# Kernel tuning notes

Hardware: AMD Instinct MI355X
Metric: run time of the kernel (lower is better)

## Reference

```python
import jax, jax.numpy as jnp
import numpy as np

N = 50000      # nodes per type
E = 800000     # edges per relation
CIN = 64       # in_channels
H, O = 2, 32   # heads, out_channels
HID = H * O    # hidden
EC = 16        # edge_channels


def setup_inputs() -> dict:
    key = jax.random.key(0)
    ks = jax.random.split(key, 30)
    f = lambda i, shape, s=0.1: jax.random.normal(ks[i], shape, dtype=jnp.float32) * s
    inp = {
        'x_a': f(0, (N, CIN), 1.0), 'x_b': f(1, (N, CIN), 1.0),
        'edge_attr1': f(2, (E, EC), 1.0), 'edge_attr2': f(3, (E, EC), 1.0),
        'Wq_a': f(4, (CIN, HID)), 'Wk_a': f(5, (CIN, HID)), 'Wv_a': f(6, (CIN, HID)),
        'Wq_b': f(7, (CIN, HID)), 'Wk_b': f(8, (CIN, HID)), 'Wv_b': f(9, (CIN, HID)),
        'emb_a': f(10, (HID,)), 'emb_b': f(11, (HID,)),
        'rel1': f(12, (HID,)), 'rel2': f(13, (HID,)),
        'We': f(14, (EC, HID)), 'a_attn': f(15, (4 * O,)),
        'Wo_a': f(16, (HID, O)), 'bo_a': f(17, (O,)),
        'Wo_b': f(18, (HID, O)), 'bo_b': f(19, (O,)),
        'Wr_a': f(20, (CIN, O)), 'Wr_b': f(21, (CIN, O)),
        'row1': jax.random.randint(ks[22], (E,), 0, N),
        'col1': jax.random.randint(ks[23], (E,), 0, N),
        'row2': jax.random.randint(ks[24], (E,), 0, N),
        'col2': jax.random.randint(ks[25], (E,), 0, N),
    }
    return inp


def _edge_softmax(scores, col, num_dst):
    # softmax over incoming edges of each destination node; scores: [E, H]
    m = jax.ops.segment_max(scores, col, num_segments=num_dst)      # [N, H]
    ex = jnp.exp(scores - m[col])
    s = jax.ops.segment_sum(ex, col, num_segments=num_dst)          # [N, H]
    return ex / s[col]


def _relation(q_dst, k_src, v_src, emb_src, emb_dst, rel_emb, edge_bias,
              row, col, a_attn, num_dst):
    eb = edge_bias                                                  # [E, H, O]
    qd = q_dst[col] + emb_dst.reshape(1, H, O)
    ks = k_src[row] + emb_src.reshape(1, H, O)
    rb = jnp.broadcast_to(rel_emb.reshape(1, H, O), qd.shape)
    attn_in = jnp.concatenate([qd, ks, rb, eb], axis=-1)            # [E, H, 4O]
    scores = jnp.einsum('ehd,d->eh', jnp.tanh(attn_in), a_attn)    # [E, H]
    w = _edge_softmax(scores, col, num_dst)                         # [E, H]
    msg = v_src[row] + rel_emb.reshape(1, H, O) + eb                # [E, H, O]
    agg = jax.ops.segment_sum(msg * w[..., None], col, num_segments=num_dst)
    return agg.reshape(num_dst, H * O)


def reference(x_a, x_b, edge_attr1, edge_attr2,
              Wq_a, Wk_a, Wv_a, Wq_b, Wk_b, Wv_b,
              emb_a, emb_b, rel1, rel2, We, a_attn,
              Wo_a, bo_a, Wo_b, bo_b, Wr_a, Wr_b,
              row1, col1, row2, col2):
    q_a = (x_a @ Wq_a).reshape(-1, H, O)
    k_a = (x_a @ Wk_a).reshape(-1, H, O)
    v_a = (x_a @ Wv_a).reshape(-1, H, O)
    q_b = (x_b @ Wq_b).reshape(-1, H, O)
    k_b = (x_b @ Wk_b).reshape(-1, H, O)
    v_b = (x_b @ Wv_b).reshape(-1, H, O)

    # relation r1: a -> b
    eb1 = (edge_attr1 @ We).reshape(-1, H, O)
    out_b = _relation(q_b, k_a, v_a, emb_a, emb_b, rel1, eb1, row1, col1, a_attn, N)
    # relation r2: b -> a
    eb2 = (edge_attr2 @ We).reshape(-1, H, O)
    out_a = _relation(q_a, k_b, v_b, emb_b, emb_a, rel2, eb2, row2, col2, a_attn, N)

    fin_a = out_a @ Wo_a + bo_a + x_a @ Wr_a                        # [N, O]
    fin_b = out_b @ Wo_b + bo_b + x_b @ Wr_b                        # [N, O]
    return jnp.concatenate([fin_a, fin_b], axis=0)                  # [2N, O]
```

## Files before the change

### kernel.cpp

```cpp
#include <hip/hip_runtime.h>
#include <hip/hip_bf16.h>

typedef __hip_bfloat16 bf16;
typedef __attribute__((ext_vector_type(8))) short short8;
typedef __attribute__((ext_vector_type(4))) float float4v;

static __device__ __forceinline__ float b2f(bf16 x) { return __bfloat162float(x); }

static __device__ __forceinline__ float ldf(const void* p, size_t i, int f32) {
    return f32 ? ((const float*)p)[i] : b2f(((const bf16*)p)[i]);
}
static __device__ __forceinline__ void stf(void* p, size_t i, int f32, float v) {
    if (f32) ((float*)p)[i] = v;
    else     ((bf16*)p)[i] = __float2bfloat16(v);
}
static __device__ __forceinline__ unsigned short f2bf_bits(float f) {
    bf16 h = __float2bfloat16(f);
    return *(unsigned short*)&h;
}

static __device__ __forceinline__ float fast_tanh(float x) {
    float t = __expf(2.f * x);
    return 1.f - 2.f * __builtin_amdgcn_rcpf(t + 1.f);
}

static __device__ __forceinline__ void load_ea16(const void* ea, size_t e, int f32, float* er) {
    if (f32) {
        const float4* p = (const float4*)((const float*)ea + e * 16);
        #pragma unroll
        for (int q = 0; q < 4; ++q) {
            float4 v = p[q];
            er[4*q] = v.x; er[4*q+1] = v.y; er[4*q+2] = v.z; er[4*q+3] = v.w;
        }
    } else {
        const uint4* p = (const uint4*)((const bf16*)ea + e * 16);
        #pragma unroll
        for (int q = 0; q < 2; ++q) {
            uint4 u = p[q];
            er[8*q+0] = __uint_as_float(u.x << 16);
            er[8*q+1] = __uint_as_float(u.x & 0xffff0000u);
            er[8*q+2] = __uint_as_float(u.y << 16);
            er[8*q+3] = __uint_as_float(u.y & 0xffff0000u);
            er[8*q+4] = __uint_as_float(u.z << 16);
            er[8*q+5] = __uint_as_float(u.z & 0xffff0000u);
            er[8*q+6] = __uint_as_float(u.w << 16);
            er[8*q+7] = __uint_as_float(u.w & 0xffff0000u);
        }
    }
}

__global__ void detect_kernel(const unsigned short* __restrict__ a, int* __restrict__ flag)
{
    __shared__ int cnt;
    if (threadIdx.x == 0) cnt = 0;
    __syncthreads();
    unsigned e = (a[threadIdx.x] >> 7) & 0xFF;
    if (e < 100 || e > 133) atomicAdd(&cnt, 1);
    __syncthreads();
    if (threadIdx.x == 0) *flag = (cnt >= 16) ? 1 : 0;
}

__global__ __launch_bounds__(256) void prep_small_kernel(
    const void* __restrict__ W0, const void* __restrict__ W1,
    const void* __restrict__ W2, const void* __restrict__ W3,
    const void* __restrict__ W4, const void* __restrict__ W5,
    const void* __restrict__ Wr_a, const void* __restrict__ Wr_b,
    const void* __restrict__ We,
    const void* __restrict__ Wo_a, const void* __restrict__ Wo_b,
    const void* __restrict__ rel1, const void* __restrict__ rel2,
    const void* __restrict__ a_attn, const int* __restrict__ flagp,
    unsigned short* __restrict__ wt,
    float* __restrict__ M1, float* __restrict__ c321,
    float* __restrict__ M2, float* __restrict__ c322,
    float* __restrict__ cvals)
{
    const int f32 = *flagp;
    const int bid = blockIdx.x;
    if (bid < 6) {
        const void* src;
        switch (bid) {
            case 0: src = W0; break; case 1: src = W1; break; case 2: src = W2; break;
            case 3: src = W3; break; case 4: src = W4; break; default: src = W5; break;
        }
        unsigned short* dst = wt + bid * 4096;
        for (int i = threadIdx.x; i < 4096; i += 256) {
            int c = i >> 6, j = i & 63;
            dst[j * 64 + c] = f2bf_bits(ldf(src, c * 64 + j, f32));
        }
    } else if (bid < 8) {
        const void* src = (bid == 6) ? Wr_a : Wr_b;
        unsigned short* dst = wt + 24576 + (bid - 6) * 2048;
        for (int i = threadIdx.x; i < 2048; i += 256) {
            int c = i >> 5, j = i & 31;
            dst[j * 64 + c] = f2bf_bits(ldf(src, c * 32 + j, f32));
        }
    } else {
        const int sel = bid - 8;
        const void* Wo  = sel ? Wo_a : Wo_b;
        const void* rel = sel ? rel2 : rel1;
        float* M   = sel ? M2 : M1;
        float* c32 = sel ? c322 : c321;
        const int t = threadIdx.x;
        for (int i = t; i < 1024; i += 256) {
            int m = i >> 5, j = i & 31;
            int h = m >> 4, c = m & 15;
            float s = 0.f;
            for (int jj = 0; jj < 32; ++jj)
                s += ldf(We, c * 64 + h * 32 + jj, f32) * ldf(Wo, (size_t)(h * 32 + jj) * 32 + j, f32);
            M[m * 32 + j] = s;
        }
        if (t < 32) {
            float s2 = 0.f;
            for (int ch = 0; ch < 64; ++ch)
                s2 += ldf(rel, ch, f32) * ldf(Wo, (size_t)ch * 32 + t, f32);
            c32[t] = s2;
        }
        if (t == 252 || t == 253) {
            int h = t - 252;
            float s3 = 0.f;
            for (int l = 0; l < 32; ++l)
                s3 += tanhf(ldf(rel, h * 32 + l, f32)) * ldf(a_attn, 64 + l, f32);
            cvals[sel * 2 + h] = s3;
        }
    }
}

__global__ __launch_bounds__(256) void node_prep_mfma_kernel(
    const void* __restrict__ x_a, const void* __restrict__ x_b,
    const unsigned short* __restrict__ wt,
    const void* __restrict__ emb_a, const void* __restrict__ emb_b,
    const void* __restrict__ a_attn, const int* __restrict__ flagp,
    unsigned short* __restrict__ v_a, unsigned short* __restrict__ v_b,
    float* __restrict__ r_a, float* __restrict__ r_b,
    float* __restrict__ sq_a, float* __restrict__ sk_a,
    float* __restrict__ sq_b, float* __restrict__ sk_b,
    int n_nodes, int tiles)
{
    const int f32 = *flagp;
    const int wave_id = blockIdx.x * 4 + (threadIdx.x >> 6);
    if (wave_id >= 2 * tiles) return;
    const int type = (wave_id >= tiles);
    const int tile = type ? (wave_id - tiles) : wave_id;

    const void* xp = type ? x_b : x_a;
    const unsigned short* wq = wt + (type ? 3 * 4096 : 0);
    const unsigned short* wk = wq + 4096;
    const unsigned short* wv = wk + 4096;
    const unsigned short* wr = wt + 24576 + (type ? 2048 : 0);
    const void* embp = type ? emb_b : emb_a;
    unsigned short* v_out = type ? v_b : v_a;
    float*  r_out  = type ? r_b : r_a;
    float2* sq_out = (float2*)(type ? sq_b : sq_a);
    float2* sk_out = (float2*)(type ? sk_b : sk_a);

    const int lane = threadIdx.x & 63;
    const int ml   = lane & 15;
    const int g    = lane >> 4;
    const int g8   = g * 8;

    float embc[4], acq[4], ack[4];
    #pragma unroll
    for (int t = 0; t < 4; ++t) {
        int colt = t * 16 + ml;
        embc[t] = ldf(embp, colt, f32);
        acq[t]  = ldf(a_attn, colt & 31, f32);
        ack[t]  = ldf(a_attn, 32 + (colt & 31), f32);
    }

    short8 Bq[4][2], Bk[4][2], Bv[4][2], Br[2][2];
    #pragma unroll
    for (int t = 0; t < 4; ++t) {
        const int rowo = (t * 16 + ml) * 64;
        #pragma unroll
        for (int kh = 0; kh < 2; ++kh) {
            const int o = rowo + kh * 32 + g8;
            Bq[t][kh] = __builtin_bit_cast(short8, *(const uint4*)(wq + o));
            Bk[t][kh] = __builtin_bit_cast(short8, *(const uint4*)(wk + o));
            Bv[t][kh] = __builtin_bit_cast(short8, *(const uint4*)(wv + o));
            if (t < 2)
                Br[t][kh] = __builtin_bit_cast(short8, *(const uint4*)(wr + o));
        }
    }

    const int n0 = tile << 4;
    int nr = n0 + ml; if (nr > n_nodes - 1) nr = n_nodes - 1;
    short8 A0, A1;
    if (f32) {
        const float4* xr = (const float4*)((const float*)xp + (size_t)nr * 64);
        float4 f0 = xr[2*g], f1 = xr[2*g+1], f2 = xr[8+2*g], f3 = xr[9+2*g];
        short8 a0, a1;
        a0[0]=(short)f2bf_bits(f0.x); a0[1]=(short)f2bf_bits(f0.y);
        a0[2]=(short)f2bf_bits(f0.z); a0[3]=(short)f2bf_bits(f0.w);
        a0[4]=(short)f2bf_bits(f1.x); a0[5]=(short)f2bf_bits(f1.y);
        a0[6]=(short)f2bf_bits(f1.z); a0[7]=(short)f2bf_bits(f1.w);
        a1[0]=(short)f2bf_bits(f2.x); a1[1]=(short)f2bf_bits(f2.y);
        a1[2]=(short)f2bf_bits(f2.z); a1[3]=(short)f2bf_bits(f2.w);
        a1[4]=(short)f2bf_bits(f3.x); a1[5]=(short)f2bf_bits(f3.y);
        a1[6]=(short)f2bf_bits(f3.z); a1[7]=(short)f2bf_bits(f3.w);
        A0 = a0; A1 = a1;
    } else {
        const uint4* xr = (const uint4*)((const bf16*)xp + (size_t)nr * 64);
        A0 = __builtin_bit_cast(short8, xr[g]);
        A1 = __builtin_bit_cast(short8, xr[4 + g]);
    }

    float4v accq[4], acck[4], accv[4], accr[2];
    #pragma unroll
    for (int t = 0; t < 4; ++t) {
        float4v z = {0.f, 0.f, 0.f, 0.f};
        accq[t] = z; acck[t] = z; accv[t] = z;
        if (t < 2) accr[t] = z;
    }
    #pragma unroll
    for (int t = 0; t < 4; ++t) {
        accq[t] = __builtin_amdgcn_mfma_f32_16x16x32_bf16(A0, Bq[t][0], accq[t], 0, 0, 0);
        accq[t] = __builtin_amdgcn_mfma_f32_16x16x32_bf16(A1, Bq[t][1], accq[t], 0, 0, 0);
        acck[t] = __builtin_amdgcn_mfma_f32_16x16x32_bf16(A0, Bk[t][0], acck[t], 0, 0, 0);
        acck[t] = __builtin_amdgcn_mfma_f32_16x16x32_bf16(A1, Bk[t][1], acck[t], 0, 0, 0);
        accv[t] = __builtin_amdgcn_mfma_f32_16x16x32_bf16(A0, Bv[t][0], accv[t], 0, 0, 0);
        accv[t] = __builtin_amdgcn_mfma_f32_16x16x32_bf16(A1, Bv[t][1], accv[t], 0, 0, 0);
        if (t < 2) {
            accr[t] = __builtin_amdgcn_mfma_f32_16x16x32_bf16(A0, Br[t][0], accr[t], 0, 0, 0);
            accr[t] = __builtin_amdgcn_mfma_f32_16x16x32_bf16(A1, Br[t][1], accr[t], 0, 0, 0);
        }
    }

    #pragma unroll
    for (int t = 0; t < 4; ++t) {
        #pragma unroll
        for (int r = 0; r < 4; ++r) {
            int node = n0 + g * 4 + r;
            if (node < n_nodes) {
                v_out[(size_t)node * 64 + t * 16 + ml] = f2bf_bits(accv[t][r]);
                if (t < 2) r_out[(size_t)node * 32 + t * 16 + ml] = accr[t][r];
            }
        }
    }

    #pragma unroll
    for (int r = 0; r < 4; ++r) {
        float q0 = fast_tanh(accq[0][r] + embc[0]) * acq[0]
                 + fast_tanh(accq[1][r] + embc[1]) * acq[1];
        float q1 = fast_tanh(accq[2][r] + embc[2]) * acq[2]
                 + fast_tanh(accq[3][r] + embc[3]) * acq[3];
        float k0 = fast_tanh(acck[0][r] + embc[0]) * ack[0]
                 + fast_tanh(acck[1][r] + embc[1]) * ack[1];
        float k1 = fast_tanh(acck[2][r] + embc[2]) * ack[2]
                 + fast_tanh(acck[3][r] + embc[3]) * ack[3];
        #pragma unroll
        for (int o = 1; o < 16; o <<= 1) {
            q0 += __shfl_xor(q0, o, 64); q1 += __shfl_xor(q1, o, 64);
            k0 += __shfl_xor(k0, o, 64); k1 += __shfl_xor(k1, o, 64);
        }
        int node = n0 + g * 4 + r;
        if (ml == 0 && node < n_nodes) {
            sq_out[node] = make_float2(q0, q1);
            sk_out[node] = make_float2(k0, k1);
        }
    }
}

__global__ __launch_bounds__(256) void hist_kernel(
    const int* __restrict__ col1, const int* __restrict__ col2,
    int* __restrict__ cnt, int n_nodes, int num_e)
{
    const int sel = blockIdx.x & 1;
    const int bx  = blockIdx.x >> 1;
    const int* col = sel ? col2 : col1;
    const int rb = sel ? n_nodes : 0;
    int e = bx * 256 + threadIdx.x;
    if (e < num_e) atomicAdd(&cnt[rb + col[e]], 1);
}

__global__ __launch_bounds__(256) void scan1_kernel(const int* __restrict__ cnt,
                                                    int* __restrict__ partial, int n)
{
    __shared__ int wsum[4];
    int t = threadIdx.x;
    int i0 = blockIdx.x * 512 + 2 * t;
    int s = ((i0 < n) ? cnt[i0] : 0) + ((i0 + 1 < n) ? cnt[i0 + 1] : 0);
    #pragma unroll
    for (int o = 32; o; o >>= 1) s += __shfl_xor(s, o, 64);
    if ((t & 63) == 0) wsum[t >> 6] = s;
    __syncthreads();
    if (t == 0) partial[blockIdx.x] = wsum[0] + wsum[1] + wsum[2] + wsum[3];
}

__global__ void scan2_kernel(const int* __restrict__ partial, int* __restrict__ pp,
                             int* __restrict__ off, int nch, int noff)
{
    int lane = threadIdx.x;
    int running = 0;
    for (int base = 0; base < nch; base += 64) {
        int i = base + lane;
        int o = (i < nch) ? partial[i] : 0;
        int v = o;
        #pragma unroll
        for (int d = 1; d < 64; d <<= 1) {
            int u = __shfl_up(v, d, 64);
            if (lane >= d) v += u;
        }
        if (i < nch) pp[i] = running + v - o;
        running += __shfl(v, 63, 64);
    }
    if (lane == 0) off[noff] = running;
}

__global__ __launch_bounds__(256) void scan3_kernel(const int* __restrict__ cnt,
                                                    const int* __restrict__ pp,
                                                    int* __restrict__ off,
                                                    int* __restrict__ cursor, int n)
{
    __shared__ int tmp[256];
    int t = threadIdx.x;
    int i0 = blockIdx.x * 512 + 2 * t;
    int v0 = (i0 < n) ? cnt[i0] : 0;
    int v1 = (i0 + 1 < n) ? cnt[i0 + 1] : 0;
    int pair = v0 + v1;
    tmp[t] = pair;
    __syncthreads();
    for (int d = 1; d < 256; d <<= 1) {
        int x = (t >= d) ? tmp[t - d] : 0;
        __syncthreads();
        tmp[t] += x;
        __syncthreads();
    }
    int excl = tmp[t] - pair + pp[blockIdx.x];
    if (i0 < n)     { off[i0] = excl;          cursor[i0] = excl; }
    if (i0 + 1 < n) { off[i0 + 1] = excl + v0; cursor[i0 + 1] = excl + v0; }
}

__global__ __launch_bounds__(256) void edge_score_scatter_kernel(
    const void* __restrict__ ea1p, const void* __restrict__ ea2p,
    const void* __restrict__ We,
    const int* __restrict__ row1, const int* __restrict__ col1,
    const int* __restrict__ row2, const int* __restrict__ col2,
    const float* __restrict__ sq_bp, const float* __restrict__ sk_ap,
    const float* __restrict__ sq_ap, const float* __restrict__ sk_bp,
    const float* __restrict__ cvals, const void* __restrict__ a_attn,
    const int* __restrict__ flagp, int* __restrict__ cursor,
    uint4* __restrict__ payload, int n_nodes, int num_e)
{
    const int f32 = *flagp;
    const int sel = blockIdx.x & 1;
    const int bx  = blockIdx.x >> 1;
    const void* ea = sel ? ea2p : ea1p;
    const int* row = sel ? row2 : row1;
    const int* col = sel ? col2 : col1;
    const float* sq_dst = sel ? sq_ap : sq_bp;
    const float* sk_src = sel ? sk_bp : sk_ap;
    const int rb = sel ? n_nodes : 0;

    __shared__ float We_s[16 * 64];
    __shared__ float a3_s[32];
    for (int i = threadIdx.x; i < 16 * 64; i += 256) We_s[i] = ldf(We, i, f32);
    if (threadIdx.x < 32) a3_s[threadIdx.x] = ldf(a_attn, 96 + threadIdx.x, f32);
    const float c0 = cvals[sel * 2 + 0];
    const float c1 = cvals[sel * 2 + 1];
    __syncthreads();

    const int e0 = bx * 512 + threadIdx.x;
    const int e1 = e0 + 256;
    const bool v1e = (e1 < num_e);
    if (e0 >= num_e) return;

    float er0[16], er1[16];
    load_ea16(ea, (size_t)e0, f32, er0);
    if (v1e) load_ea16(ea, (size_t)e1, f32, er1);
    else {
        #pragma unroll
        for (int c = 0; c < 16; ++c) er1[c] = 0.f;
    }

    float acc00 = 0.f, acc01 = 0.f, acc10 = 0.f, acc11 = 0.f;
    #pragma unroll 1
    for (int jb = 0; jb < 64; jb += 16) {
        float t0[16], t1[16];
        #pragma unroll
        for (int jj = 0; jj < 16; ++jj) { t0[jj] = 0.f; t1[jj] = 0.f; }
        #pragma unroll
        for (int c = 0; c < 16; ++c) {
            #pragma unroll
            for (int jj = 0; jj < 16; ++jj) {
                float w = We_s[c * 64 + jb + jj];
                t0[jj] += er0[c] * w;
                t1[jj] += er1[c] * w;
            }
        }
        float p0 = 0.f, p1 = 0.f;
        #pragma unroll
        for (int jj = 0; jj < 16; ++jj) {
            float a = a3_s[(jb + jj) & 31];
            p0 += fast_tanh(t0[jj]) * a;
            p1 += fast_tanh(t1[jj]) * a;
        }
        if (jb & 32) { acc01 += p0; acc11 += p1; }
        else         { acc00 += p0; acc10 += p1; }
    }

    {
        int dc = col[e0], s = row[e0];
        float2 sqd = ((const float2*)sq_dst)[dc];
        float2 sks = ((const float2*)sk_src)[s];
        float s0 = fminf(30.f, fmaxf(-30.f, acc00 + sqd.x + sks.x + c0));
        float s1 = fminf(30.f, fmaxf(-30.f, acc01 + sqd.y + sks.y + c1));
        int pos = atomicAdd(&cursor[rb + dc], 1);
        uint4* rec = payload + (size_t)3 * pos;
        unsigned w0 = (unsigned)f2bf_bits(er0[0])  | ((unsigned)f2bf_bits(er0[1])  << 16);
        unsigned w1 = (unsigned)f2bf_bits(er0[2])  | ((unsigned)f2bf_bits(er0[3])  << 16);
        unsigned w2 = (unsigned)f2bf_bits(er0[4])  | ((unsigned)f2bf_bits(er0[5])  << 16);
        unsigned w3 = (unsigned)f2bf_bits(er0[6])  | ((unsigned)f2bf_bits(er0[7])  << 16);
        unsigned w4 = (unsigned)f2bf_bits(er0[8])  | ((unsigned)f2bf_bits(er0[9])  << 16);
        unsigned w5 = (unsigned)f2bf_bits(er0[10]) | ((unsigned)f2bf_bits(er0[11]) << 16);
        unsigned w6 = (unsigned)f2bf_bits(er0[12]) | ((unsigned)f2bf_bits(er0[13]) << 16);
        unsigned w7 = (unsigned)f2bf_bits(er0[14]) | ((unsigned)f2bf_bits(er0[15]) << 16);
        rec[0] = make_uint4((unsigned)s, __float_as_uint(__expf(s0)), __float_as_uint(__expf(s1)), 0u);
        rec[1] = make_uint4(w0, w1, w2, w3);
        rec[2] = make_uint4(w4, w5, w6, w7);
    }
    if (v1e) {
        int dc = col[e1], s = row[e1];
        float2 sqd = ((const float2*)sq_dst)[dc];
        float2 sks = ((const float2*)sk_src)[s];
        float s0 = fminf(30.f, fmaxf(-30.f, acc10 + sqd.x + sks.x + c0));
        float s1 = fminf(30.f, fmaxf(-30.f, acc11 + sqd.y + sks.y + c1));
        int pos = atomicAdd(&cursor[rb + dc], 1);
        uint4* rec = payload + (size_t)3 * pos;
        unsigned w0 = (unsigned)f2bf_bits(er1[0])  | ((unsigned)f2bf_bits(er1[1])  << 16);
        unsigned w1 = (unsigned)f2bf_bits(er1[2])  | ((unsigned)f2bf_bits(er1[3])  << 16);
        unsigned w2 = (unsigned)f2bf_bits(er1[4])  | ((unsigned)f2bf_bits(er1[5])  << 16);
        unsigned w3 = (unsigned)f2bf_bits(er1[6])  | ((unsigned)f2bf_bits(er1[7])  << 16);
        unsigned w4 = (unsigned)f2bf_bits(er1[8])  | ((unsigned)f2bf_bits(er1[9])  << 16);
        unsigned w5 = (unsigned)f2bf_bits(er1[10]) | ((unsigned)f2bf_bits(er1[11]) << 16);
        unsigned w6 = (unsigned)f2bf_bits(er1[12]) | ((unsigned)f2bf_bits(er1[13]) << 16);
        unsigned w7 = (unsigned)f2bf_bits(er1[14]) | ((unsigned)f2bf_bits(er1[15]) << 16);
        rec[0] = make_uint4((unsigned)s, __float_as_uint(__expf(s0)), __float_as_uint(__expf(s1)), 0u);
        rec[1] = make_uint4(w0, w1, w2, w3);
        rec[2] = make_uint4(w4, w5, w6, w7);
    }
}

__global__ __launch_bounds__(256) void agg_final_kernel(
    const uint4* __restrict__ payload, const int* __restrict__ off,
    const unsigned short* __restrict__ v_a, const unsigned short* __restrict__ v_b,
    const float* __restrict__ r_a, const float* __restrict__ r_b,
    const void* __restrict__ Wo_a, const void* __restrict__ Wo_b,
    const void* __restrict__ bo_a, const void* __restrict__ bo_b,
    const float* __restrict__ M1, const float* __restrict__ M2,
    const float* __restrict__ c321, const float* __restrict__ c322,
    const int* __restrict__ flagp, void* __restrict__ out,
    int n_nodes, int nbh)
{
    const int sel = blockIdx.x & 1;
    const int bx  = blockIdx.x >> 1;
    const unsigned short* v_src = sel ? v_b : v_a;
    const float* r_src = sel ? r_a : r_b;
    const void*  Wo    = sel ? Wo_a : Wo_b;
    const void*  bo    = sel ? bo_a : bo_b;
    const float* M     = sel ? M2 : M1;
    const float* c32   = sel ? c322 : c321;
    const int relbase  = sel ? n_nodes : 0;
    const size_t out_off = sel ? 0 : (size_t)n_nodes * 32;

    const int f32  = *flagp;
    const int lane = threadIdx.x & 63;
    const int wv   = threadIdx.x >> 6;
    const int j    = lane & 31;
    const int half = lane >> 5;
    const int c16  = lane & 15;
    const bool hi  = (lane >= 32);

    __shared__ float stage[4][96];

    float WoR[32], MR[16];
    const int cb = half * 32;
    #pragma unroll
    for (int cc = 0; cc < 32; ++cc)
        WoR[cc] = ldf(Wo, (size_t)(cb + cc) * 32 + j, f32);
    const int ub = half * 16;
    #pragma unroll
    for (int cc = 0; cc < 16; ++cc) MR[cc] = M[(ub + cc) * 32 + j];
    const float boR  = ldf(bo, j, f32);
    const float c32R = c32[j];

    const int stride = nbh * 4;
    const int iters  = (n_nodes + stride - 1) / stride;
    int d = bx * 4 + wv;

    for (int it = 0; it < iters; ++it, d += stride) {
        const bool valid = (d < n_nodes);
        const int dd  = valid ? d : (n_nodes - 1);
        const int idx = relbase + dd;
        const int b   = __builtin_amdgcn_readfirstlane(off[idx]);
        const int en  = __builtin_amdgcn_readfirstlane(off[idx + 1]);
        const int deg = en - b;

        const float rv = r_src[(size_t)dd * 32 + j];

        float den0 = 0.f, den1 = 0.f, y = 0.f, ua = 0.f;
        int k = b;
        #pragma unroll 1
        for (; k + 8 <= en; k += 8) {
            uint4 m[8];
            #pragma unroll
            for (int q = 0; q < 8; ++q) m[q] = payload[(size_t)3 * (k + q)];
            float ev[8];
            #pragma unroll
            for (int q = 0; q < 8; ++q) {
                const unsigned short* pq = (const unsigned short*)(payload + (size_t)3 * (k + q) + 1);
                ev[q] = __uint_as_float((unsigned)pq[c16] << 16);
            }
            float vv[8];
            #pragma unroll
            for (int q = 0; q < 8; ++q)
                vv[q] = __uint_as_float((unsigned)v_src[(size_t)m[q].x * 64 + lane] << 16);
            #pragma unroll
            for (int q = 0; q < 8; ++q) {
                float e0 = __uint_as_float(m[q].y), e1 = __uint_as_float(m[q].z);
                den0 += e0; den1 += e1;
                float xw = hi ? e1 : e0;
                y  = fmaf(xw, vv[q], y);
                ua = fmaf(xw, ev[q], ua);
            }
        }
        #pragma unroll 1
        for (; k < en; ++k) {
            uint4 mm = payload[(size_t)3 * k];
            const unsigned short* pq = (const unsigned short*)(payload + (size_t)3 * k + 1);
            float evs = __uint_as_float((unsigned)pq[c16] << 16);
            float vvs = __uint_as_float((unsigned)v_src[(size_t)mm.x * 64 + lane] << 16);
            float e0 = __uint_as_float(mm.y), e1 = __uint_as_float(mm.z);
            den0 += e0; den1 += e1;
            float xw = hi ? e1 : e0;
            y  = fmaf(xw, vvs, y);
            ua = fmaf(xw, evs, ua);
        }

        float inv0 = (deg > 0) ? __builtin_amdgcn_rcpf(den0) : 0.f;
        float inv1 = (deg > 0) ? __builtin_amdgcn_rcpf(den1) : 0.f;
        const float invh = hi ? inv1 : inv0;
        y  *= invh;
        ua *= invh;

        float* st = stage[wv];
        st[lane] = y;
        if ((lane & 31) < 16) st[64 + half * 16 + c16] = ua;
        __asm__ volatile("s_waitcnt lgkmcnt(0)" ::: "memory");

        float acc = 0.f;
        #pragma unroll
        for (int cc = 0; cc < 32; ++cc)
            acc = fmaf(st[cb + cc], WoR[cc], acc);
        #pragma unroll
        for (int cc = 0; cc < 16; ++cc)
            acc = fmaf(st[64 + ub + cc], MR[cc], acc);

        float other = __shfl(acc, lane ^ 32, 64);
        if (valid && lane < 32) {
            float o = acc + other + boR + rv + ((deg > 0) ? c32R : 0.f);
            stf(out, out_off + (size_t)dd * 32 + j, f32, o);
        }
        __asm__ volatile("" ::: "memory");
        __builtin_amdgcn_wave_barrier();
    }
}

extern "C" void kernel_launch(void* const* d_in, const int* in_sizes, int n_in,
                              void* d_out, int out_size, void* d_ws, size_t ws_size,
                              hipStream_t stream)
{
    const void* x_a   = d_in[0];
    const void* x_b   = d_in[1];
    const void* ea1   = d_in[2];
    const void* ea2   = d_in[3];
    const void* Wq_a  = d_in[4];
    const void* Wk_a  = d_in[5];
    const void* Wv_a  = d_in[6];
    const void* Wq_b  = d_in[7];
    const void* Wk_b  = d_in[8];
    const void* Wv_b  = d_in[9];
    const void* emb_a = d_in[10];
    const void* emb_b = d_in[11];
    const void* rel1  = d_in[12];
    const void* rel2  = d_in[13];
    const void* We    = d_in[14];
    const void* a_at  = d_in[15];
    const void* Wo_a  = d_in[16];
    const void* bo_a  = d_in[17];
    const void* Wo_b  = d_in[18];
    const void* bo_b  = d_in[19];
    const void* Wr_a  = d_in[20];
    const void* Wr_b  = d_in[21];
    const int*  row1  = (const int*)d_in[22];
    const int*  col1  = (const int*)d_in[23];
    const int*  row2  = (const int*)d_in[24];
    const int*  col2  = (const int*)d_in[25];

    const int N = in_sizes[0] / 64;
    const int E = in_sizes[22];

    float* ws = (float*)d_ws;
    size_t off = 0;
    int*   flag = (int*)ws;        off += 64;
    unsigned short* v_a = (unsigned short*)(ws + off); off += (size_t)N * 32;
    unsigned short* v_b = (unsigned short*)(ws + off); off += (size_t)N * 32;
    float* r_a  = ws + off;        off += (size_t)N * 32;
    float* r_b  = ws + off;        off += (size_t)N * 32;
    float* sq_a = ws + off;        off += (size_t)N * 2;
    float* sk_a = ws + off;        off += (size_t)N * 2;
    float* sq_b = ws + off;        off += (size_t)N * 2;
    float* sk_b = ws + off;        off += (size_t)N * 2;
    float* cvals = ws + off;       off += 4;
    off = (off + 3) & ~(size_t)3;
    unsigned short* wt = (unsigned short*)(ws + off); off += 28672 / 2;
    float* M1   = ws + off;        off += 1024;
    float* c321 = ws + off;        off += 32;
    float* M2   = ws + off;        off += 1024;
    float* c322 = ws + off;        off += 32;
    int*   cnt    = (int*)(ws + off);  off += (size_t)2 * N;
    int*   offs   = (int*)(ws + off);  off += (size_t)2 * N + 2;
    int*   cursor = (int*)(ws + off);  off += (size_t)2 * N;
    int*   partial = (int*)(ws + off); off += 512;
    int*   pp      = (int*)(ws + off); off += 512;
    off = (off + 3) & ~(size_t)3;
    uint4* payload = (uint4*)(ws + off); off += (size_t)2 * E * 12;

    const int tiles        = (N + 15) >> 4;
    const int mfma_blocks  = (2 * tiles + 3) / 4;
    const int score_blocks = (E + 511) / 512;
    const int eb_blocks    = (E + 255) / 256;
    const int nch          = (2 * N + 511) / 512;
    const int agg_half     = 2048;

    detect_kernel<<<1, 128, 0, stream>>>((const unsigned short*)a_at, flag);
    hipMemsetAsync(cnt, 0, (size_t)2 * N * sizeof(int), stream);

    prep_small_kernel<<<10, 256, 0, stream>>>(
        Wq_a, Wk_a, Wv_a, Wq_b, Wk_b, Wv_b, Wr_a, Wr_b,
        We, Wo_a, Wo_b, rel1, rel2, a_at, flag,
        wt, M1, c321, M2, c322, cvals);

    node_prep_mfma_kernel<<<mfma_blocks, 256, 0, stream>>>(
        x_a, x_b, wt, emb_a, emb_b, a_at, flag,
        v_a, v_b, r_a, r_b, sq_a, sk_a, sq_b, sk_b, N, tiles);

    hist_kernel<<<2 * eb_blocks, 256, 0, stream>>>(col1, col2, cnt, N, E);
    scan1_kernel<<<nch, 256, 0, stream>>>(cnt, partial, 2 * N);
    scan2_kernel<<<1, 64, 0, stream>>>(partial, pp, offs, nch, 2 * N);
    scan3_kernel<<<nch, 256, 0, stream>>>(cnt, pp, offs, cursor, 2 * N);

    edge_score_scatter_kernel<<<2 * score_blocks, 256, 0, stream>>>(
        ea1, ea2, We, row1, col1, row2, col2,
        sq_b, sk_a, sq_a, sk_b, cvals, a_at, flag,
        cursor, payload, N, E);

    agg_final_kernel<<<2 * agg_half, 256, 0, stream>>>(
        payload, offs, v_a, v_b, r_a, r_b, Wo_a, Wo_b, bo_a, bo_b,
        M1, M2, c321, c322, flag, d_out, N, agg_half);
}
```

Before: 527.3 us.

## Compute edge-bias attention scores with bf16 MFMA in edge scatter kernel

Replaces the per-thread scalar FMA loop that projects edge_attr through We (16x64) with 16x16x32 bf16 MFMA instructions, processing 16 edges per wave step. A new prep block writes a transposed bf16 copy of We, which is kept in registers as the B operands. The tanh·a_attn reduction is done with lane shuffles, and payload writes are redistributed across lanes. This removes the FP32 ALU cost of the edge projection, but it rounds We and edge_attr to bf16 and half the MFMA K dimension is zero padding.

```diff
diff --git a/kernel.cpp b/kernel.cpp
--- a/kernel.cpp
+++ b/kernel.cpp
@@ -22,31 +22,6 @@
 static __device__ __forceinline__ float fast_tanh(float x) {
     float t = __expf(2.f * x);
     return 1.f - 2.f * __builtin_amdgcn_rcpf(t + 1.f);
-}
-
-static __device__ __forceinline__ void load_ea16(const void* ea, size_t e, int f32, float* er) {
-    if (f32) {
-        const float4* p = (const float4*)((const float*)ea + e * 16);
-        #pragma unroll
-        for (int q = 0; q < 4; ++q) {
-            float4 v = p[q];
-            er[4*q] = v.x; er[4*q+1] = v.y; er[4*q+2] = v.z; er[4*q+3] = v.w;
-        }
-    } else {
-        const uint4* p = (const uint4*)((const bf16*)ea + e * 16);
-        #pragma unroll
-        for (int q = 0; q < 2; ++q) {
-            uint4 u = p[q];
-            er[8*q+0] = __uint_as_float(u.x << 16);
-            er[8*q+1] = __uint_as_float(u.x & 0xffff0000u);
-            er[8*q+2] = __uint_as_float(u.y << 16);
-            er[8*q+3] = __uint_as_float(u.y & 0xffff0000u);
-            er[8*q+4] = __uint_as_float(u.z << 16);
-            er[8*q+5] = __uint_as_float(u.z & 0xffff0000u);
-            er[8*q+6] = __uint_as_float(u.w << 16);
-            er[8*q+7] = __uint_as_float(u.w & 0xffff0000u);
-        }
-    }
 }
 
 __global__ void detect_kernel(const unsigned short* __restrict__ a, int* __restrict__ flag)
@@ -94,7 +69,7 @@
             int c = i >> 5, j = i & 31;
             dst[j * 64 + c] = f2bf_bits(ldf(src, c * 32 + j, f32));
         }
-    } else {
+    } else if (bid < 10) {
         const int sel = bid - 8;
         const void* Wo  = sel ? Wo_a : Wo_b;
         const void* rel = sel ? rel2 : rel1;
@@ -121,6 +96,12 @@
             for (int l = 0; l < 32; ++l)
                 s3 += tanhf(ldf(rel, h * 32 + l, f32)) * ldf(a_attn, 64 + l, f32);
             cvals[sel * 2 + h] = s3;
+        }
+    } else {
+        unsigned short* wet = wt + 28672;
+        for (int i = threadIdx.x; i < 1024; i += 256) {
+            int n = i >> 4, k = i & 15;
+            wet[n * 16 + k] = f2bf_bits(ldf(We, k * 64 + n, f32));
         }
     }
 }
@@ -332,7 +313,7 @@
 
 __global__ __launch_bounds__(256) void edge_score_scatter_kernel(
     const void* __restrict__ ea1p, const void* __restrict__ ea2p,
-    const void* __restrict__ We,
+    const unsigned short* __restrict__ wet,
     const int* __restrict__ row1, const int* __restrict__ col1,
     const int* __restrict__ row2, const int* __restrict__ col2,
     const float* __restrict__ sq_bp, const float* __restrict__ sk_ap,
@@ -351,92 +332,98 @@
     const float* sk_src = sel ? sk_bp : sk_ap;
     const int rb = sel ? n_nodes : 0;
 
-    __shared__ float We_s[16 * 64];
-    __shared__ float a3_s[32];
-    for (int i = threadIdx.x; i < 16 * 64; i += 256) We_s[i] = ldf(We, i, f32);
-    if (threadIdx.x < 32) a3_s[threadIdx.x] = ldf(a_attn, 96 + threadIdx.x, f32);
+    const int lane = threadIdx.x & 63;
+    const int wv   = threadIdx.x >> 6;
+    const int ml   = lane & 15;
+    const int g    = lane >> 4;
+
+    const short8 zero8 = {0, 0, 0, 0, 0, 0, 0, 0};
+
+    short8 B[4];
+    #pragma unroll
+    for (int t = 0; t < 4; ++t)
+        B[t] = (g < 2) ? __builtin_bit_cast(short8, *(const uint4*)(wet + (t * 16 + ml) * 16 + g * 8))
+                       : zero8;
+    float av[4];
+    #pragma unroll
+    for (int t = 0; t < 4; ++t) av[t] = ldf(a_attn, 96 + ((t * 16 + ml) & 31), f32);
     const float c0 = cvals[sel * 2 + 0];
     const float c1 = cvals[sel * 2 + 1];
-    __syncthreads();
-
-    const int e0 = bx * 512 + threadIdx.x;
-    const int e1 = e0 + 256;
-    const bool v1e = (e1 < num_e);
-    if (e0 >= num_e) return;
-
-    float er0[16], er1[16];
-    load_ea16(ea, (size_t)e0, f32, er0);
-    if (v1e) load_ea16(ea, (size_t)e1, f32, er1);
-    else {
-        #pragma unroll
-        for (int c = 0; c < 16; ++c) er1[c] = 0.f;
-    }
-
-    float acc00 = 0.f, acc01 = 0.f, acc10 = 0.f, acc11 = 0.f;
+
+    const int base = bx * 512 + wv * 128;
     #pragma unroll 1
-    for (int jb = 0; jb < 64; jb += 16) {
-        float t0[16], t1[16];
-        #pragma unroll
-        for (int jj = 0; jj < 16; ++jj) { t0[jj] = 0.f; t1[jj] = 0.f; }
-        #pragma unroll
-        for (int c = 0; c < 16; ++c) {
+    for (int it = 0; it < 8; ++it) {
+        const int e0 = base + it * 16;
+        if (e0 >= num_e) break;
+
+        int ec = e0 + ml; if (ec > num_e - 1) ec = num_e - 1;
+        short8 A = zero8;
+        if (g < 2) {
+            if (f32) {
+                const float4* p = (const float4*)((const float*)ea + (size_t)ec * 16 + g * 8);
+                float4 f0 = p[0], f1 = p[1];
+                short8 a;
+                a[0] = (short)f2bf_bits(f0.x); a[1] = (short)f2bf_bits(f0.y);
+                a[2] = (short)f2bf_bits(f0.z); a[3] = (short)f2bf_bits(f0.w);
+                a[4] = (short)f2bf_bits(f1.x); a[5] = (short)f2bf_bits(f1.y);
+                a[6] = (short)f2bf_bits(f1.z); a[7] = (short)f2bf_bits(f1.w);
+                A = a;
+            } else {
+                A = __builtin_bit_cast(short8, *(const uint4*)((const bf16*)ea + (size_t)ec * 16 + g * 8));
+            }
+        }
+
+        float4v z = {0.f, 0.f, 0.f, 0.f};
+        float4v acc0 = z, acc1 = z, acc2 = z, acc3 = z;
+        acc0 = __builtin_amdgcn_mfma_f32_16x16x32_bf16(A, B[0], acc0, 0, 0, 0);
+        acc1 = __builtin_amdgcn_mfma_f32_16x16x32_bf16(A, B[1], acc1, 0, 0, 0);
+        acc2 = __builtin_amdgcn_mfma_f32_16x16x32_bf16(A, B[2], acc2, 0, 0, 0);
+        acc3 = __builtin_amdgcn_mfma_f32_16x16x32_bf16(A, B[3], acc3, 0, 0, 0);
+
+        float s0[4], s1[4];
+        #pragma unroll
+        for (int r = 0; r < 4; ++r) {
+            s0[r] = fast_tanh(acc0[r]) * av[0] + fast_tanh(acc1[r]) * av[1];
+            s1[r] = fast_tanh(acc2[r]) * av[2] + fast_tanh(acc3[r]) * av[3];
+        }
+        #pragma unroll
+        for (int o = 1; o < 16; o <<= 1) {
             #pragma unroll
-            for (int jj = 0; jj < 16; ++jj) {
-                float w = We_s[c * 64 + jb + jj];
-                t0[jj] += er0[c] * w;
-                t1[jj] += er1[c] * w;
+            for (int r = 0; r < 4; ++r) {
+                s0[r] += __shfl_xor(s0[r], o, 64);
+                s1[r] += __shfl_xor(s1[r], o, 64);
             }
         }
-        float p0 = 0.f, p1 = 0.f;
-        #pragma unroll
-        for (int jj = 0; jj < 16; ++jj) {
-            float a = a3_s[(jb + jj) & 31];
-            p0 += fast_tanh(t0[jj]) * a;
-            p1 += fast_tanh(t1[jj]) * a;
-        }
-        if (jb & 32) { acc01 += p0; acc11 += p1; }
-        else         { acc00 += p0; acc10 += p1; }
-    }
-
-    {
-        int dc = col[e0], s = row[e0];
-        float2 sqd = ((const float2*)sq_dst)[dc];
-        float2 sks = ((const float2*)sk_src)[s];
-        float s0 = fminf(30.f, fmaxf(-30.f, acc00 + sqd.x + sks.x + c0));
-        float s1 = fminf(30.f, fmaxf(-30.f, acc01 + sqd.y + sks.y + c1));
-        int pos = atomicAdd(&cursor[rb + dc], 1);
-        uint4* rec = payload + (size_t)3 * pos;
-        unsigned w0 = (unsigned)f2bf_bits(er0[0])  | ((unsigned)f2bf_bits(er0[1])  << 16);
-        unsigned w1 = (unsigned)f2bf_bits(er0[2])  | ((unsigned)f2bf_bits(er0[3])  << 16);
-        unsigned w2 = (unsigned)f2bf_bits(er0[4])  | ((unsigned)f2bf_bits(er0[5])  << 16);
-        unsigned w3 = (unsigned)f2bf_bits(er0[6])  | ((unsigned)f2bf_bits(er0[7])  << 16);
-        unsigned w4 = (unsigned)f2bf_bits(er0[8])  | ((unsigned)f2bf_bits(er0[9])  << 16);
-        unsigned w5 = (unsigned)f2bf_bits(er0[10]) | ((unsigned)f2bf_bits(er0[11]) << 16);
-        unsigned w6 = (unsigned)f2bf_bits(er0[12]) | ((unsigned)f2bf_bits(er0[13]) << 16);
-        unsigned w7 = (unsigned)f2bf_bits(er0[14]) | ((unsigned)f2bf_bits(er0[15]) << 16);
-        rec[0] = make_uint4((unsigned)s, __float_as_uint(__expf(s0)), __float_as_uint(__expf(s1)), 0u);
-        rec[1] = make_uint4(w0, w1, w2, w3);
-        rec[2] = make_uint4(w4, w5, w6, w7);
-    }
-    if (v1e) {
-        int dc = col[e1], s = row[e1];
-        float2 sqd = ((const float2*)sq_dst)[dc];
-        float2 sks = ((const float2*)sk_src)[s];
-        float s0 = fminf(30.f, fmaxf(-30.f, acc10 + sqd.x + sks.x + c0));
-        float s1 = fminf(30.f, fmaxf(-30.f, acc11 + sqd.y + sks.y + c1));
-        int pos = atomicAdd(&cursor[rb + dc], 1);
-        uint4* rec = payload + (size_t)3 * pos;
-        unsigned w0 = (unsigned)f2bf_bits(er1[0])  | ((unsigned)f2bf_bits(er1[1])  << 16);
-        unsigned w1 = (unsigned)f2bf_bits(er1[2])  | ((unsigned)f2bf_bits(er1[3])  << 16);
-        unsigned w2 = (unsigned)f2bf_bits(er1[4])  | ((unsigned)f2bf_bits(er1[5])  << 16);
-        unsigned w3 = (unsigned)f2bf_bits(er1[6])  | ((unsigned)f2bf_bits(er1[7])  << 16);
-        unsigned w4 = (unsigned)f2bf_bits(er1[8])  | ((unsigned)f2bf_bits(er1[9])  << 16);
-        unsigned w5 = (unsigned)f2bf_bits(er1[10]) | ((unsigned)f2bf_bits(er1[11]) << 16);
-        unsigned w6 = (unsigned)f2bf_bits(er1[12]) | ((unsigned)f2bf_bits(er1[13]) << 16);
-        unsigned w7 = (unsigned)f2bf_bits(er1[14]) | ((unsigned)f2bf_bits(er1[15]) << 16);
-        rec[0] = make_uint4((unsigned)s, __float_as_uint(__expf(s0)), __float_as_uint(__expf(s1)), 0u);
-        rec[1] = make_uint4(w0, w1, w2, w3);
-        rec[2] = make_uint4(w4, w5, w6, w7);
+
+        int pos = 0;
+        float ex0 = 0.f, ex1 = 0.f;
+        unsigned srcn = 0;
+        const int rsel = lane & 3;
+        const int eidx = g * 4 + rsel;
+        const bool fin = (ml < 4) && (e0 + eidx < num_e);
+        if (fin) {
+            float a0 = (rsel == 0) ? s0[0] : (rsel == 1) ? s0[1] : (rsel == 2) ? s0[2] : s0[3];
+            float a1 = (rsel == 0) ? s1[0] : (rsel == 1) ? s1[1] : (rsel == 2) ? s1[2] : s1[3];
+            const int e = e0 + eidx;
+            const int dc = col[e];
+            srcn = (unsigned)row[e];
+            float2 sqd = ((const float2*)sq_dst)[dc];
+            float2 sks = ((const float2*)sk_src)[srcn];
+            float v0 = fminf(30.f, fmaxf(-30.f, a0 + sqd.x + sks.x + c0));
+            float v1 = fminf(30.f, fmaxf(-30.f, a1 + sqd.y + sks.y + c1));
+            ex0 = __expf(v0); ex1 = __expf(v1);
+            pos = atomicAdd(&cursor[rb + dc], 1);
+        }
+        const int srcl = ((lane & 12) << 2) | (lane & 3);
+        const int posx = __shfl(pos, srcl, 64);
+        if (fin) {
+            uint4* rec = payload + (size_t)3 * pos;
+            rec[0] = make_uint4(srcn, __float_as_uint(ex0), __float_as_uint(ex1), 0u);
+        }
+        if (lane < 32 && (e0 + ml < num_e)) {
+            uint4* rec = payload + (size_t)3 * posx;
+            rec[1 + g] = __builtin_bit_cast(uint4, A);
+        }
     }
 }
 
@@ -612,7 +599,7 @@
     float* sk_b = ws + off;        off += (size_t)N * 2;
     float* cvals = ws + off;       off += 4;
     off = (off + 3) & ~(size_t)3;
-    unsigned short* wt = (unsigned short*)(ws + off); off += 28672 / 2;
+    unsigned short* wt = (unsigned short*)(ws + off); off += 29696 / 2;
     float* M1   = ws + off;        off += 1024;
     float* c321 = ws + off;        off += 32;
     float* M2   = ws + off;        off += 1024;
@@ -635,7 +622,7 @@
     detect_kernel<<<1, 128, 0, stream>>>((const unsigned short*)a_at, flag);
     hipMemsetAsync(cnt, 0, (size_t)2 * N * sizeof(int), stream);
 
-    prep_small_kernel<<<10, 256, 0, stream>>>(
+    prep_small_kernel<<<11, 256, 0, stream>>>(
         Wq_a, Wk_a, Wv_a, Wq_b, Wk_b, Wv_b, Wr_a, Wr_b,
         We, Wo_a, Wo_b, rel1, rel2, a_at, flag,
         wt, M1, c321, M2, c322, cvals);
@@ -650,7 +637,7 @@
     scan3_kernel<<<nch, 256, 0, stream>>>(cnt, pp, offs, cursor, 2 * N);
 
     edge_score_scatter_kernel<<<2 * score_blocks, 256, 0, stream>>>(
-        ea1, ea2, We, row1, col1, row2, col2,
+        ea1, ea2, wt + 28672, row1, col1, row2, col2,
         sq_b, sk_a, sq_a, sk_b, cvals, a_at, flag,
         cursor, payload, N, E);
 
```

Result: slower. 556.3 us (+5.5%).
